# Kernel tuning notes

Hardware: AMD Instinct MI355X
Metric: run time of the kernel (lower is better)

Reference implementation:

```python
import jax, jax.numpy as jnp
import numpy as np

B, N, D = 2, 2048, 256
H = 8
HD = D // H
SCALE = HD ** 0.5  # NOTE: source MULTIPLIES by sqrt(head_dim)
EPS = 1e-5
DFF = 4 * D


def setup_inputs() -> dict:
    key = jax.random.key(0)
    ks = jax.random.split(key, 9)
    s = lambda fan_in: 1.0 / np.sqrt(fan_in)
    return {
        "x": jax.random.normal(ks[0], (B, N, D), dtype=jnp.float32),
        # weights stored [in, out] (transposed torch Linear)
        "qkv_w": jax.random.normal(ks[1], (D, 3 * D), dtype=jnp.float32) * s(D),
        "proj_w": jax.random.normal(ks[2], (D, D), dtype=jnp.float32) * s(D),
        "proj_b": jax.random.normal(ks[3], (D,), dtype=jnp.float32) * 0.01,
        "fc1_w": jax.random.normal(ks[4], (D, DFF), dtype=jnp.float32) * s(D),
        "fc1_b": jax.random.normal(ks[5], (DFF,), dtype=jnp.float32) * 0.01,
        "fc2_w": jax.random.normal(ks[6], (DFF, D), dtype=jnp.float32) * s(DFF),
        "fc2_b": jax.random.normal(ks[7], (D,), dtype=jnp.float32) * 0.01,
        "ln1_g": jnp.ones((D,), dtype=jnp.float32),
        "ln1_b": jnp.zeros((D,), dtype=jnp.float32),
    }


def _layernorm(x, g, b):
    mu = jnp.mean(x, axis=-1, keepdims=True)
    var = jnp.mean(jnp.square(x - mu), axis=-1, keepdims=True)
    return (x - mu) * jax.lax.rsqrt(var + EPS) * g + b


def reference(x, qkv_w, proj_w, proj_b, fc1_w, fc1_b, fc2_w, fc2_b, ln1_g, ln1_b):
    b, n, d = x.shape
    # --- MHA ---
    qkv = (x @ qkv_w).reshape(b, n, 3, H, HD)
    q = qkv[:, :, 0].transpose(0, 2, 1, 3)  # [B,H,N,HD]
    k = qkv[:, :, 1].transpose(0, 2, 1, 3)
    v = qkv[:, :, 2].transpose(0, 2, 1, 3)
    att = jnp.einsum("bhqd,bhkd->bhqk", q, k) * SCALE  # multiplied, per source
    att = jax.nn.softmax(att, axis=-1)
    out = jnp.einsum("bhqk,bhkd->bhqd", att, v)
    out = out.transpose(0, 2, 1, 3).reshape(b, n, d)
    out = out @ proj_w + proj_b
    # --- post-norm residual ---
    net = _layernorm(out + x, ln1_g, ln1_b)
    shortcut = net
    # --- MLP (NO activation in source forward) ---
    net = (net @ fc1_w + fc1_b) @ fc2_w + fc2_b
    return net + shortcut
```

## Files before the change

### kernel.cpp

```cpp
#include <hip/hip_runtime.h>


typedef __attribute__((ext_vector_type(8))) short short8;
typedef __attribute__((ext_vector_type(8))) _Float16 half8;
typedef __attribute__((ext_vector_type(4))) _Float16 half4;
typedef __attribute__((ext_vector_type(2))) __fp16 fp16x2;
typedef __attribute__((ext_vector_type(4))) float floatx4;
typedef __attribute__((ext_vector_type(2))) unsigned int uint2v;
typedef unsigned short u16;

#define MFMAG(a,b,c)  __builtin_amdgcn_mfma_f32_16x16x32_f16((a),(b),(c),0,0,0)
#if __has_builtin(__builtin_amdgcn_mfma_f32_16x16x16_f16)
#define MFMAPV(a,b,c) __builtin_amdgcn_mfma_f32_16x16x16_f16((a),(b),(c),0,0,0)
#else
#define MFMAPV(a,b,c) __builtin_amdgcn_mfma_f32_16x16x16f16((a),(b),(c),0,0,0)
#endif
#define CLF 8.1615404f

#if __has_builtin(__builtin_amdgcn_exp2f)
#define EX2(x) __builtin_amdgcn_exp2f(x)
#else
#define EX2(x) exp2f(x)
#endif

__device__ __forceinline__ float bf2f(u16 u) { return __uint_as_float(((unsigned)u) << 16); }
__device__ __forceinline__ float h2f(u16 u) { _Float16 h = *(_Float16*)&u; return (float)h; }
__device__ __forceinline__ u16 f2h(float f) { _Float16 h = (_Float16)f; return *(u16*)&h; }
__device__ __forceinline__ unsigned pkh2(float a, float b) {
#if __has_builtin(__builtin_amdgcn_cvt_pkrtz)
  fp16x2 h = __builtin_amdgcn_cvt_pkrtz(a, b);
  return *(unsigned*)&h;
#else
  return (unsigned)f2h(a) | ((unsigned)f2h(b) << 16);
#endif
}
__device__ __forceinline__ void gll16(const void* g, void* l) {
  __builtin_amdgcn_global_load_lds((const __attribute__((address_space(1))) void*)g,
                                   (__attribute__((address_space(3))) void*)l, 16, 0, 0);
}

__global__ __launch_bounds__(256) void prep_k(
    const void* __restrict__ x, const void* __restrict__ qkv_w,
    const void* __restrict__ proj_w, const void* __restrict__ fc1_w,
    const void* __restrict__ fc2_w, const void* __restrict__ proj_b,
    const void* __restrict__ fc1_b, const void* __restrict__ fc2_b,
    const void* __restrict__ ln_g, const void* __restrict__ ln_b,
    u16* __restrict__ x_f, u16* __restrict__ wq_f,
    u16* __restrict__ wt_proj, u16* __restrict__ wt_fc1, u16* __restrict__ wt_fc2,
    u16* __restrict__ b_proj, u16* __restrict__ b_fc1, u16* __restrict__ b_fc2,
    u16* __restrict__ g_ln, u16* __restrict__ bb_ln)
{
  const int lane = threadIdx.x & 63;
  const float probe = bf2f(((const u16*)qkv_w)[lane]);
  const bool f32 = __ballot(!(fabsf(probe) < 1000.0f)) != 0ull;
  const int bid = blockIdx.x, tid = threadIdx.x;
  #define RD(p, i) (f32 ? ((const float*)(p))[i] : bf2f(((const u16*)(p))[i]))
  if (bid < 4096) {
    const size_t i = (size_t)bid * 256 + tid;
    x_f[i] = f2h(RD(x, i));
  } else if (bid < 4864) {
    const int idx = (bid - 4096) * 256 + tid;
    const int n = idx >> 8, k = idx & 255;
    wq_f[idx] = f2h(RD(qkv_w, (size_t)k * 768 + n));
  } else if (bid < 5120) {
    const int idx = (bid - 4864) * 256 + tid;
    wt_proj[idx] = f2h(RD(proj_w, (size_t)(idx & 255) * 256 + (idx >> 8)));
  } else if (bid < 6144) {
    const int idx = (bid - 5120) * 256 + tid;
    wt_fc1[idx] = f2h(RD(fc1_w, (size_t)(idx & 255) * 1024 + (idx >> 8)));
  } else if (bid < 7168) {
    const int idx = (bid - 6144) * 256 + tid;
    wt_fc2[idx] = f2h(RD(fc2_w, (size_t)(idx & 1023) * 256 + (idx >> 10)));
  } else {
    const int j = (bid - 7168) * 256 + tid;
    if (j < 256)       b_proj[j]        = f2h(RD(proj_b, j));
    else if (j < 1280) b_fc1[j - 256]   = f2h(RD(fc1_b, j - 256));
    else if (j < 1536) b_fc2[j - 1280]  = f2h(RD(fc2_b, j - 1280));
    else if (j < 1792) g_ln[j - 1536]   = f2h(RD(ln_g, j - 1536));
    else               bb_ln[j - 1792]  = f2h(RD(ln_b, j - 1792));
  }
  #undef RD
}

template<int TW, int EPI, bool BIAS, bool RES, bool COMB>
__global__ __launch_bounds__(256) void gemm_k(
    const u16* __restrict__ A, const u16* __restrict__ Bt, const u16* __restrict__ A2,
    const u16* __restrict__ bias, const u16* __restrict__ res,
    void* __restrict__ out0, u16* __restrict__ aux1, u16* __restrict__ aux3,
    const float* __restrict__ muc,
    int M, int Nn, int K)
{
  constexpr int BT = TW * 32;
  constexpr int NC = TW / 2;
  __shared__ __align__(16) u16 As[BT][40];
  __shared__ __align__(16) u16 Bs[BT][40];
  __shared__ __align__(16) u16 Vt[(EPI == 2) ? 64 * 72 : 1];
  const int tid = threadIdx.x;
  const int m0 = blockIdx.y * BT, n0 = blockIdx.x * BT;
  const int wid = tid >> 6, lane = tid & 63;
  const int wm = (wid >> 1) * (TW * 16), wn = (wid & 1) * (TW * 16);
  const int lm = lane & 15, quad = lane >> 4;

  floatx4 zero = {0.f, 0.f, 0.f, 0.f};
  floatx4 acc[TW][TW];
#pragma unroll
  for (int i = 0; i < TW; ++i)
#pragma unroll
    for (int j = 0; j < TW; ++j) acc[i][j] = zero;

  auto comb8 = [&](int t, int col8) -> short8 {
    const size_t o = (size_t)t * 256 + col8;
    const int h = col8 >> 5;
    const float m0_ = muc[t * 8 + h],          m1_ = muc[32768 + t * 8 + h];
    const float m2_ = muc[65536 + t * 8 + h],  m3_ = muc[98304 + t * 8 + h];
    const float M = fmaxf(fmaxf(m0_, m1_), fmaxf(m2_, m3_));
    float w0 = EX2(m0_ - M), w1 = EX2(m1_ - M), w2 = EX2(m2_ - M), w3 = EX2(m3_ - M);
    const float inv = 1.f / (w0 + w1 + w2 + w3);
    w0 *= inv; w1 *= inv; w2 *= inv; w3 *= inv;
    short8 a0 = *(const short8*)&A[o],  a1 = *(const short8*)&A[o + 1048576];
    short8 a2 = *(const short8*)&A2[o], a3 = *(const short8*)&A2[o + 1048576];
    float v[8];
#pragma unroll
    for (int j = 0; j < 8; ++j)
      v[j] = w0 * h2f((u16)a0[j]) + w1 * h2f((u16)a1[j])
           + w2 * h2f((u16)a2[j]) + w3 * h2f((u16)a3[j]);
    uint2v uu0 = {pkh2(v[0], v[1]), pkh2(v[2], v[3])};
    uint2v uu1 = {pkh2(v[4], v[5]), pkh2(v[6], v[7])};
    short8 r;
    *(uint2v*)&r = uu0; *((uint2v*)&r + 1) = uu1;
    return r;
  };

  int srow[NC], soff[NC];
#pragma unroll
  for (int c = 0; c < NC; ++c) {
    const int cid = tid * NC + c;
    srow[c] = cid >> 2; soff[c] = (cid & 3) * 8;
  }
  short8 ra[NC], rb[NC];
#pragma unroll
  for (int c = 0; c < NC; ++c) {
    rb[c] = *(const short8*)&Bt[(size_t)(n0 + srow[c]) * K + soff[c]];
    if (COMB) ra[c] = comb8(m0 + srow[c], soff[c]);
    else      ra[c] = *(const short8*)&A[(size_t)(m0 + srow[c]) * K + soff[c]];
  }
  for (int k0 = 0; k0 < K; k0 += 32) {
    if (k0) __syncthreads();
#pragma unroll
    for (int c = 0; c < NC; ++c) {
      *(short8*)&As[srow[c]][soff[c]] = ra[c];
      *(short8*)&Bs[srow[c]][soff[c]] = rb[c];
    }
    __syncthreads();
    if (k0 + 32 < K) {
#pragma unroll
      for (int c = 0; c < NC; ++c) {
        rb[c] = *(const short8*)&Bt[(size_t)(n0 + srow[c]) * K + k0 + 32 + soff[c]];
        if (COMB) ra[c] = comb8(m0 + srow[c], k0 + 32 + soff[c]);
        else      ra[c] = *(const short8*)&A[(size_t)(m0 + srow[c]) * K + k0 + 32 + soff[c]];
      }
    }
    half8 fa[TW], fb[TW];
#pragma unroll
    for (int t = 0; t < TW; ++t) {
      fa[t] = *(const half8*)&As[wm + t * 16 + lm][quad * 8];
      fb[t] = *(const half8*)&Bs[wn + t * 16 + lm][quad * 8];
    }
#pragma unroll
    for (int i = 0; i < TW; ++i)
#pragma unroll
      for (int j = 0; j < TW; ++j)
        acc[i][j] = MFMAG(fa[i], fb[j], acc[i][j]);
  }

  if (EPI == 2 && n0 >= 512) {
    __syncthreads();
#pragma unroll
    for (int i = 0; i < TW; ++i)
#pragma unroll
      for (int j = 0; j < TW; ++j)
#pragma unroll
        for (int r = 0; r < 4; ++r)
          Vt[(wn + j * 16 + lm) * 72 + wm + i * 16 + quad * 4 + r] = f2h(acc[i][j][r]);
    __syncthreads();
    const int bb = m0 >> 11, n = m0 & 2047;
#pragma unroll
    for (int pass = 0; pass < 2; ++pass) {
      const int dl = (tid >> 3) + pass * 32;
      const int oct = tid & 7;
      const int col = n0 - 512 + dl;
      const int d = col & 31, hh = col >> 5;
      short8 v = *(const short8*)&Vt[dl * 72 + oct * 8];
      *(short8*)&((u16*)out0)[(size_t)((bb * 8 + hh) * 32 + d) * 2048 + n + oct * 8] = v;
    }
    return;
  }

#pragma unroll
  for (int i = 0; i < TW; ++i) {
    const int rowb = m0 + wm + i * 16 + quad * 4;
#pragma unroll
    for (int j = 0; j < TW; ++j) {
      const int col = n0 + wn + j * 16 + lm;
      const float bv = BIAS ? h2f(bias[col]) : 0.f;
#pragma unroll
      for (int r = 0; r < 4; ++r) {
        const int row = rowb + r;
        float v = acc[i][j][r] + bv;
        const size_t o = (size_t)row * Nn + col;
        if (RES) v += h2f(res[o]);
        if (EPI == 0) {
          ((float*)out0)[o] = v;
        } else if (EPI == 1) {
          ((u16*)out0)[o] = f2h(v);
        } else {
          if (col < 256) aux1[(size_t)row * 256 + col] = f2h(v);
          else           aux3[(size_t)row * 256 + (col - 256)] = f2h(v);
        }
      }
    }
  }
}

template<int CHUNKS>
__global__ __launch_bounds__(256) void attn_k(
    const u16* __restrict__ qf16, const u16* __restrict__ kf16,
    const u16* __restrict__ vt, u16* __restrict__ outp, u16* __restrict__ out23,
    float* __restrict__ mu)
{
  __shared__ __align__(16) u16 Ks[2][64][32];
  __shared__ __align__(16) u16 Vs[2][32][64];
  const int tid = threadIdx.x, wid = tid >> 6, lane = tid & 63;
  const int lm = lane & 15, quad = lane >> 4;
  const int bid = blockIdx.x;
  const int chunk = (CHUNKS > 1) ? (bid >> 9) : 0;
  const int qblk = bid & 31, bh = (bid >> 5) & 15;
  const int b = bh >> 3, h = bh & 7;
  const int q0 = qblk * 64 + wid * 16;
  const size_t tb = (size_t)b * 2048;
  const int NT = 32 / CHUNKS;
  const int kofs = chunk * (2048 / CHUNKS);

  half8 qh;
  { size_t off = (tb + q0 + lm) * 256 + h * 32 + quad * 8;
    qh = *(const half8*)&qf16[off]; }

  const int kkey = tid >> 2, kg = tid & 3;
  const size_t kb = (tb + kofs + kkey) * 256 + h * 32 + kg * 8;
  const int vd = tid >> 3, vp = tid & 7, vk8 = vp ^ (vd & 7);
  const size_t vb = (size_t)(bh * 32 + vd) * 2048 + kofs + vk8 * 8;

  gll16(kf16 + kb, (u16*)Ks + tid * 8);
  gll16(vt  + vb,  (u16*)Vs + tid * 8);

  float mrun = -1e30f, lrun = 0.f;
  floatx4 o0 = {0.f,0.f,0.f,0.f}, o1 = {0.f,0.f,0.f,0.f};

  for (int kt = 0; kt < NT; ++kt) {
    const int buf = kt & 1;
    __syncthreads();
    if (kt < NT - 1) {
      const int nb = (buf ^ 1) * 2048;
      const size_t ko = (size_t)(kt + 1) * 16384;
      const size_t vo = (size_t)(kt + 1) * 64;
      gll16(kf16 + kb + ko, (u16*)Ks + nb + tid * 8);
      gll16(vt  + vb + vo,  (u16*)Vs + nb + tid * 8);
    }

    floatx4 z[4];
#pragma unroll
    for (int kf = 0; kf < 4; ++kf) {
      half8 khf = *(const half8*)&Ks[buf][kf * 16 + lm][quad * 8];
      floatx4 zz = {0.f,0.f,0.f,0.f};
      z[kf] = MFMAG(khf, qh, zz);
    }
    float zm = fmaxf(fmaxf(fmaxf(z[0][0], z[0][1]), fmaxf(z[0][2], z[0][3])),
               fmaxf(fmaxf(z[1][0], z[1][1]), fmaxf(z[1][2], z[1][3])));
    zm = fmaxf(zm, fmaxf(fmaxf(fmaxf(z[2][0], z[2][1]), fmaxf(z[2][2], z[2][3])),
                   fmaxf(fmaxf(z[3][0], z[3][1]), fmaxf(z[3][2], z[3][3]))));
    zm = fmaxf(zm, __shfl_xor(zm, 16));
    zm = fmaxf(zm, __shfl_xor(zm, 32));
    const float mn = fmaxf(mrun, zm);
    const float alpha = EX2((mrun - mn) * CLF);
    const float mc = mn * CLF;
    mrun = mn;
    float ls = 0.f;
    half4 pb[4];
#pragma unroll
    for (int kf = 0; kf < 4; ++kf) {
      const float p0 = EX2(__builtin_fmaf(z[kf][0], CLF, -mc));
      const float p1 = EX2(__builtin_fmaf(z[kf][1], CLF, -mc));
      const float p2 = EX2(__builtin_fmaf(z[kf][2], CLF, -mc));
      const float p3 = EX2(__builtin_fmaf(z[kf][3], CLF, -mc));
      ls += (p0 + p1) + (p2 + p3);
      uint2v uu = {pkh2(p0, p1), pkh2(p2, p3)};
      pb[kf] = *(half4*)&uu;
    }
    ls += __shfl_xor(ls, 16);
    ls += __shfl_xor(ls, 32);
    lrun = lrun * alpha + ls;
#pragma unroll
    for (int r = 0; r < 4; ++r) { o0[r] *= alpha; o1[r] *= alpha; }
    const u16* vbase = (const u16*)Vs + buf * 2048;
#pragma unroll
    for (int kf = 0; kf < 4; ++kf) {
      const int k8 = 2 * kf + (quad >> 1);
      const int d0 = lm, d1 = 16 + lm;
      half4 vf0 = *(const half4*)(vbase + (d0 * 8 + (k8 ^ (d0 & 7))) * 8 + (quad & 1) * 4);
      half4 vf1 = *(const half4*)(vbase + (d1 * 8 + (k8 ^ (d1 & 7))) * 8 + (quad & 1) * 4);
      o0 = MFMAPV(vf0, pb[kf], o0);
      o1 = MFMAPV(vf1, pb[kf], o1);
    }
  }
  const float inv = 1.0f / lrun;
  const size_t tok = tb + q0 + lm;
  u16* dst = ((CHUNKS > 2 && chunk >= 2) ? out23 : outp) + (size_t)(chunk & 1) * 1048576;
  const size_t rowo = tok * 256 + h * 32;
#pragma unroll
  for (int r = 0; r < 4; ++r) {
    dst[rowo + quad * 4 + r]      = f2h(o0[r] * inv);
    dst[rowo + 16 + quad * 4 + r] = f2h(o1[r] * inv);
  }
  if (CHUNKS > 1 && quad == 0)
    mu[chunk * 32768 + tok * 8 + h] = __builtin_fmaf(mrun, CLF, __log2f(lrun));
}

template<int CHUNKS>
__global__ __launch_bounds__(256) void combine_k(u16* __restrict__ d,
                                                 const u16* __restrict__ e,
                                                 const float* __restrict__ mu)
{
  const int t = blockIdx.x, c = threadIdx.x, h = c >> 5;
  const size_t o = (size_t)t * 256 + c;
  float m[CHUNKS];
  float M = -1e30f;
#pragma unroll
  for (int i = 0; i < CHUNKS; ++i) { m[i] = mu[i * 32768 + t * 8 + h]; M = fmaxf(M, m[i]); }
  float wsum = 0.f, acc = 0.f;
#pragma unroll
  for (int i = 0; i < CHUNKS; ++i) {
    const float w = EX2(m[i] - M);
    const u16 v = (i < 2) ? d[o + (size_t)i * 1048576] : e[o + (size_t)(i - 2) * 1048576];
    wsum += w; acc += w * h2f(v);
  }
  d[o] = f2h(acc / wsum);
}

__global__ __launch_bounds__(256) void ln_k(const float* __restrict__ pf,
                                            const u16* __restrict__ xh,
                                            const u16* __restrict__ g,
                                            const u16* __restrict__ bta,
                                            u16* __restrict__ net)
{
  const int t = blockIdx.x, c = threadIdx.x;
  const size_t o = (size_t)t * 256 + c;
  float v = pf[o] + h2f(xh[o]);
  float s = v, s2 = v * v;
#pragma unroll
  for (int d = 1; d < 64; d <<= 1) { s += __shfl_xor(s, d); s2 += __shfl_xor(s2, d); }
  __shared__ float ss[4], ss2[4];
  const int w = c >> 6;
  if ((c & 63) == 0) { ss[w] = s; ss2[w] = s2; }
  __syncthreads();
  s = ss[0] + ss[1] + ss[2] + ss[3];
  s2 = ss2[0] + ss2[1] + ss2[2] + ss2[3];
  const float mu = s * (1.f / 256.f);
  const float var = s2 * (1.f / 256.f) - mu * mu;
  const float is = rsqrtf(var + 1e-5f);
  net[o] = f2h((v - mu) * is * h2f(g[c]) + h2f(bta[c]));
}

extern "C" void kernel_launch(void* const* d_in, const int* in_sizes, int n_in,
                              void* d_out, int out_size, void* d_ws, size_t ws_size,
                              hipStream_t stream) {
  const void* x      = d_in[0];
  const void* qkv_w  = d_in[1];
  const void* proj_w = d_in[2];
  const void* proj_b = d_in[3];
  const void* fc1_w  = d_in[4];
  const void* fc1_b  = d_in[5];
  const void* fc2_w  = d_in[6];
  const void* fc2_b  = d_in[7];
  const void* ln_g   = d_in[8];
  const void* ln_b   = d_in[9];

  char* ws = (char*)d_ws;
  u16* b_proj  = (u16*)(ws + 4096);
  u16* b_fc1   = (u16*)(ws + 8192);
  u16* b_fc2   = (u16*)(ws + 12288);
  u16* g_ln    = (u16*)(ws + 16384);
  u16* bb_ln   = (u16*)(ws + 20480);
  u16* wq_f    = (u16*)(ws + 131072);
  u16* wt_proj = (u16*)(ws + 524288);
  u16* wt_fc1  = (u16*)(ws + 655360);
  u16* wt_fc2  = (u16*)(ws + 1179648);
  u16* x_f     = (u16*)(ws + 2097152);
  u16* q_f16   = (u16*)(ws + 4194304);
  u16* k_f16   = (u16*)(ws + 6291456);
  u16* vt      = (u16*)(ws + 8388608);
  float* mu    = (float*)(ws + 10485760);
  u16* out23   = (u16*)(ws + 11010048);
  u16* attn    = (u16*)d_out;
  float* projf = (float*)(ws + 4194304);
  u16* net     = (u16*)(ws + 11010048);
  u16* hbuf    = (u16*)(ws + 2097152);

  const bool sk4 = ws_size >= 15204352;
  const bool sk2 = ws_size >= 11010048;

  prep_k<<<7176, 256, 0, stream>>>(x, qkv_w, proj_w, fc1_w, fc2_w,
                                   proj_b, fc1_b, fc2_b, ln_g, ln_b,
                                   x_f, wq_f, wt_proj, wt_fc1, wt_fc2,
                                   b_proj, b_fc1, b_fc2, g_ln, bb_ln);

  gemm_k<2, 2, false, false, false><<<dim3(12, 64), 256, 0, stream>>>(
      x_f, wq_f, nullptr, nullptr, nullptr, vt, q_f16, k_f16, nullptr, 4096, 768, 256);
  if (sk4) {
    attn_k<4><<<2048, 256, 0, stream>>>(q_f16, k_f16, vt, attn, out23, mu);
    gemm_k<2, 0, true, false, true><<<dim3(4, 64), 256, 0, stream>>>(
        attn, wt_proj, out23, b_proj, nullptr, projf, nullptr, nullptr, mu, 4096, 256, 256);
  } else if (sk2) {
    attn_k<2><<<1024, 256, 0, stream>>>(q_f16, k_f16, vt, attn, nullptr, mu);
    combine_k<2><<<4096, 256, 0, stream>>>(attn, nullptr, mu);
    gemm_k<2, 0, true, false, false><<<dim3(4, 64), 256, 0, stream>>>(
        attn, wt_proj, nullptr, b_proj, nullptr, projf, nullptr, nullptr, nullptr,
        4096, 256, 256);
  } else {
    attn_k<1><<<512, 256, 0, stream>>>(q_f16, k_f16, vt, attn, nullptr, nullptr);
    gemm_k<2, 0, true, false, false><<<dim3(4, 64), 256, 0, stream>>>(
        attn, wt_proj, nullptr, b_proj, nullptr, projf, nullptr, nullptr, nullptr,
        4096, 256, 256);
  }
  ln_k<<<4096, 256, 0, stream>>>(projf, x_f, g_ln, bb_ln, net);
  gemm_k<2, 1, true, false, false><<<dim3(16, 64), 256, 0, stream>>>(
      net, wt_fc1, nullptr, b_fc1, nullptr, hbuf, nullptr, nullptr, nullptr,
      4096, 1024, 256);
  gemm_k<2, 0, true, true, false><<<dim3(4, 64), 256, 0, stream>>>(
      hbuf, wt_fc2, nullptr, b_fc2, net, d_out, nullptr, nullptr, nullptr,
      4096, 256, 1024);
}
```

Baseline: 149.7 us.

## Fuse split-attention combine, output projection, residual and LayerNorm into one kernel

In the four-chunk path, the separate projection GEMM (which wrote fp32 projf) and the LayerNorm kernel are replaced by a single projln_k kernel. It merges the four attention partials, multiplies by the projection weights, adds bias and residual, and applies LayerNorm in-block over full 256-wide rows. This removes one launch and an fp32 intermediate round trip through memory. In exchange the fused kernel uses only 256 blocks of 16 rows with single-buffered staging, and workspace buffers are reassigned (net aliases x_f).

```diff
diff --git a/kernel.cpp b/kernel.cpp
--- a/kernel.cpp
+++ b/kernel.cpp
@@ -222,6 +222,128 @@
   }
 }
 
+__global__ __launch_bounds__(256) void projln_k(
+    const u16* __restrict__ A,
+    const u16* __restrict__ A2,
+    const u16* __restrict__ Bt,
+    const u16* __restrict__ bias,
+    const u16* xh,
+    const u16* __restrict__ g, const u16* __restrict__ bb,
+    const float* __restrict__ muc,
+    u16* net)
+{
+  __shared__ __align__(16) u16 As[16][40];
+  __shared__ __align__(16) u16 Bs[256][40];
+  __shared__ float ss[4][16], ssq[4][16];
+  const int tid = threadIdx.x;
+  const int m0 = blockIdx.x * 16;
+  const int wid = tid >> 6, lane = tid & 63;
+  const int lm = lane & 15, quad = lane >> 4;
+
+  floatx4 zero = {0.f, 0.f, 0.f, 0.f};
+  floatx4 acc[4] = {zero, zero, zero, zero};
+
+  auto comb8 = [&](int t, int col8) -> short8 {
+    const size_t o = (size_t)t * 256 + col8;
+    const int h = col8 >> 5;
+    const float m0_ = muc[t * 8 + h],          m1_ = muc[32768 + t * 8 + h];
+    const float m2_ = muc[65536 + t * 8 + h],  m3_ = muc[98304 + t * 8 + h];
+    const float M = fmaxf(fmaxf(m0_, m1_), fmaxf(m2_, m3_));
+    float w0 = EX2(m0_ - M), w1 = EX2(m1_ - M), w2 = EX2(m2_ - M), w3 = EX2(m3_ - M);
+    const float inv = 1.f / (w0 + w1 + w2 + w3);
+    w0 *= inv; w1 *= inv; w2 *= inv; w3 *= inv;
+    short8 a0 = *(const short8*)&A[o],  a1 = *(const short8*)&A[o + 1048576];
+    short8 a2 = *(const short8*)&A2[o], a3 = *(const short8*)&A2[o + 1048576];
+    float v[8];
+#pragma unroll
+    for (int j = 0; j < 8; ++j)
+      v[j] = w0 * h2f((u16)a0[j]) + w1 * h2f((u16)a1[j])
+           + w2 * h2f((u16)a2[j]) + w3 * h2f((u16)a3[j]);
+    uint2v uu0 = {pkh2(v[0], v[1]), pkh2(v[2], v[3])};
+    uint2v uu1 = {pkh2(v[4], v[5]), pkh2(v[6], v[7])};
+    short8 r;
+    *(uint2v*)&r = uu0; *((uint2v*)&r + 1) = uu1;
+    return r;
+  };
+
+  const int arow = lane >> 2, aoff = (lane & 3) * 8;
+  int browv[4];
+#pragma unroll
+  for (int c = 0; c < 4; ++c) browv[c] = wid * 64 + c * 16 + (lane >> 2);
+  const int boff = (lane & 3) * 8;
+
+  short8 ra; short8 rb[4];
+  if (wid == 0) ra = comb8(m0 + arow, aoff);
+#pragma unroll
+  for (int c = 0; c < 4; ++c)
+    rb[c] = *(const short8*)&Bt[(size_t)browv[c] * 256 + boff];
+
+  for (int k0 = 0; k0 < 256; k0 += 32) {
+    if (k0) __syncthreads();
+    if (wid == 0) *(short8*)&As[arow][aoff] = ra;
+#pragma unroll
+    for (int c = 0; c < 4; ++c)
+      *(short8*)&Bs[browv[c]][boff] = rb[c];
+    __syncthreads();
+    if (k0 + 32 < 256) {
+      if (wid == 0) ra = comb8(m0 + arow, k0 + 32 + aoff);
+#pragma unroll
+      for (int c = 0; c < 4; ++c)
+        rb[c] = *(const short8*)&Bt[(size_t)browv[c] * 256 + k0 + 32 + boff];
+    }
+    half8 fa = *(const half8*)&As[lm][quad * 8];
+    half8 fb[4];
+#pragma unroll
+    for (int j = 0; j < 4; ++j)
+      fb[j] = *(const half8*)&Bs[wid * 64 + j * 16 + lm][quad * 8];
+#pragma unroll
+    for (int j = 0; j < 4; ++j)
+      acc[j] = MFMAG(fa, fb[j], acc[j]);
+  }
+
+  const int colb = wid * 64 + lm;
+  float s[4] = {0.f, 0.f, 0.f, 0.f}, sq[4] = {0.f, 0.f, 0.f, 0.f};
+  float vout[4][4];
+#pragma unroll
+  for (int j = 0; j < 4; ++j) {
+    const int col = colb + j * 16;
+    const float bv = h2f(bias[col]);
+#pragma unroll
+    for (int r = 0; r < 4; ++r) {
+      const int row = quad * 4 + r;
+      float v = acc[j][r] + bv + h2f(xh[(size_t)(m0 + row) * 256 + col]);
+      vout[j][r] = v;
+      s[r] += v; sq[r] += v * v;
+    }
+  }
+#pragma unroll
+  for (int d = 1; d < 16; d <<= 1)
+#pragma unroll
+    for (int r = 0; r < 4; ++r) {
+      s[r] += __shfl_xor(s[r], d);
+      sq[r] += __shfl_xor(sq[r], d);
+    }
+  if (lm == 0)
+#pragma unroll
+    for (int r = 0; r < 4; ++r) { ss[wid][quad * 4 + r] = s[r]; ssq[wid][quad * 4 + r] = sq[r]; }
+  __syncthreads();
+#pragma unroll
+  for (int r = 0; r < 4; ++r) {
+    const int row = quad * 4 + r;
+    const float ts = ss[0][row] + ss[1][row] + ss[2][row] + ss[3][row];
+    const float tq = ssq[0][row] + ssq[1][row] + ssq[2][row] + ssq[3][row];
+    const float mean = ts * (1.f / 256.f);
+    const float var = tq * (1.f / 256.f) - mean * mean;
+    const float is = rsqrtf(var + 1e-5f);
+#pragma unroll
+    for (int j = 0; j < 4; ++j) {
+      const int col = colb + j * 16;
+      net[(size_t)(m0 + row) * 256 + col] =
+          f2h((vout[j][r] - mean) * is * h2f(g[col]) + h2f(bb[col]));
+    }
+  }
+}
+
 template<int CHUNKS>
 __global__ __launch_bounds__(256) void attn_k(
     const u16* __restrict__ qf16, const u16* __restrict__ kf16,
@@ -401,6 +523,10 @@
   float* mu    = (float*)(ws + 10485760);
   u16* out23   = (u16*)(ws + 11010048);
   u16* attn    = (u16*)d_out;
+
+  u16* net4    = x_f;
+  u16* hbuf4   = (u16*)(ws + 4194304);
+
   float* projf = (float*)(ws + 4194304);
   u16* net     = (u16*)(ws + 11010048);
   u16* hbuf    = (u16*)(ws + 2097152);
@@ -417,9 +543,17 @@
       x_f, wq_f, nullptr, nullptr, nullptr, vt, q_f16, k_f16, nullptr, 4096, 768, 256);
   if (sk4) {
     attn_k<4><<<2048, 256, 0, stream>>>(q_f16, k_f16, vt, attn, out23, mu);
-    gemm_k<2, 0, true, false, true><<<dim3(4, 64), 256, 0, stream>>>(
-        attn, wt_proj, out23, b_proj, nullptr, projf, nullptr, nullptr, mu, 4096, 256, 256);
-  } else if (sk2) {
+    projln_k<<<256, 256, 0, stream>>>(attn, out23, wt_proj, b_proj, x_f,
+                                      g_ln, bb_ln, mu, net4);
+    gemm_k<2, 1, true, false, false><<<dim3(16, 64), 256, 0, stream>>>(
+        net4, wt_fc1, nullptr, b_fc1, nullptr, hbuf4, nullptr, nullptr, nullptr,
+        4096, 1024, 256);
+    gemm_k<2, 0, true, true, false><<<dim3(4, 64), 256, 0, stream>>>(
+        hbuf4, wt_fc2, nullptr, b_fc2, net4, d_out, nullptr, nullptr, nullptr,
+        4096, 256, 1024);
+    return;
+  }
+  if (sk2) {
     attn_k<2><<<1024, 256, 0, stream>>>(q_f16, k_f16, vt, attn, nullptr, mu);
     combine_k<2><<<4096, 256, 0, stream>>>(attn, nullptr, mu);
     gemm_k<2, 0, true, false, false><<<dim3(4, 64), 256, 0, stream>>>(
```

Result: faster. 143.8 us (-3.9%).
